# Kernel optimization log

Hardware: AMD Instinct MI355X
Metric: run time of the kernel (lower is better)

Reference implementation:

```python
import jax, jax.numpy as jnp
import numpy as np

INPUT_DIM = 128
RESERVOIR = 4096
SR = 0.95
SCALE_IN = 1.0
LEAK = 0.3
DENSITY = 0.1
T = 2048


def setup_inputs() -> dict:
    key = jax.random.key(0)
    kx, kin, kw, km = jax.random.split(key, 4)
    x = jax.random.normal(kx, (T, INPUT_DIM), dtype=jnp.float32)
    # input weights ~ U(-scale_in, scale_in)
    W_in = jax.random.uniform(kin, (RESERVOIR, INPUT_DIM), minval=-SCALE_IN, maxval=SCALE_IN, dtype=jnp.float32)
    # sparse recurrent weights ~ U(-1,1) with given density, rescaled to target
    # spectral radius via circular-law estimate rho ~= sqrt(N * density * Var),
    # Var(U(-1,1)) = 1/3 (avoids an O(N^3) eig at setup; same math structure).
    W_dense = jax.random.uniform(kw, (RESERVOIR, RESERVOIR), minval=-1.0, maxval=1.0, dtype=jnp.float32)
    mask = (jax.random.uniform(km, (RESERVOIR, RESERVOIR)) < DENSITY).astype(jnp.float32)
    rho_est = float(np.sqrt(RESERVOIR * DENSITY / 3.0))
    W = W_dense * mask * (SR / rho_est)
    return {"x": x, "W_in": W_in, "W": W}


def reference(x, W_in, W):
    # Leaky-integrator ESN: h_t = (1-a) h_{t-1} + a * tanh(W_in x_t + W h_{t-1})
    a = jnp.float32(LEAK)
    h0 = jnp.zeros((W.shape[0],), dtype=x.dtype)

    def step(h, xt):
        pre = W_in @ xt + W @ h
        h_new = (1.0 - a) * h + a * jnp.tanh(pre)
        return h_new, h_new

    _, states = jax.lax.scan(step, h0, x)
    # torch.stack(states) -> [T, reservoir]
    return states
```

## Files before the change

kernel.cpp:

```cpp
#include <hip/hip_runtime.h>

#define N 4096
#define IN_DIM 128
#define T_STEPS 2048
#define KSLOTS 576
#define CHUNKS (KSLOTS / 64)
#define NBLOCKS 256
#define NTHREADS 512
#define ROWS_PER_WAVE 2
#define ROWS_PER_BLOCK (ROWS_PER_WAVE * (NTHREADS / 64))
#define SENTINEL_BITS 0x7FC00001u

typedef float f32x4 __attribute__((ext_vector_type(4)));

__global__ void init_sentinel(float* __restrict__ out) {
    const size_t i = (size_t)blockIdx.x * blockDim.x + threadIdx.x;
    __hip_atomic_store(&out[i], __uint_as_float(SENTINEL_BITS),
                       __ATOMIC_RELAXED, __HIP_MEMORY_SCOPE_AGENT);
}

__global__ void build_ell(const float* __restrict__ W,
                          float* __restrict__ vals,
                          unsigned short* __restrict__ cols) {
    __shared__ float sval[KSLOTS];
    __shared__ unsigned short scol[KSLOTS];
    __shared__ float slot_val[KSLOTS];
    __shared__ unsigned short slot_col[KSLOTS];
    __shared__ int chunk_fill[CHUNKS];
    __shared__ int cnt;

    const int r = blockIdx.x;
    const int tid = threadIdx.x;
    if (tid == 0) cnt = 0;
    if (tid < CHUNKS) chunk_fill[tid] = 0;
    __syncthreads();

    const float* wrow = W + (size_t)r * N;
    for (int j = tid; j < N; j += blockDim.x) {
        float w = wrow[j];
        if (w != 0.0f) {
            int p = atomicAdd(&cnt, 1);
            if (p < KSLOTS) { sval[p] = w; scol[p] = (unsigned short)j; }
        }
    }
    __syncthreads();
    for (int j = tid; j < KSLOTS; j += blockDim.x) { slot_val[j] = 0.0f; slot_col[j] = 0; }
    __syncthreads();

    if (tid < 32) {
        int k = 0;
        const int n = (cnt < KSLOTS) ? cnt : KSLOTS;
        for (int p = 0; p < n; ++p) {
            int c = scol[p];
            if ((c & 31) == tid) {
                int ch0 = (k + tid) % CHUNKS;
                for (int probe = 0; probe < CHUNKS; ++probe) {
                    int cc = ch0 + probe; if (cc >= CHUNKS) cc -= CHUNKS;
                    int pos = atomicAdd(&chunk_fill[cc], 1);
                    if (pos < 64) {
                        slot_val[cc * 64 + pos] = sval[p];
                        slot_col[cc * 64 + pos] = (unsigned short)c;
                        break;
                    }
                }
                ++k;
            }
        }
    }
    __syncthreads();

    float* vrow = vals + (size_t)r * KSLOTS;
    unsigned short* crow = cols + (size_t)r * KSLOTS;
    for (int j = tid; j < KSLOTS; j += blockDim.x) { vrow[j] = slot_val[j]; crow[j] = slot_col[j]; }
}

__device__ __forceinline__ f32x4 load_coherent_x4(const float* p) {
    f32x4 v;
    asm volatile("global_load_dwordx4 %0, %1, off sc0 sc1\n\t"
                 "s_waitcnt vmcnt(0)"
                 : "=v"(v) : "v"(p) : "memory");
    return v;
}

__device__ __forceinline__ void load_coherent_x4_pair(const float* p0, const float* p1,
                                                      f32x4* v0, f32x4* v1) {
    f32x4 a, b;
    asm volatile("global_load_dwordx4 %0, %2, off sc0 sc1\n\t"
                 "global_load_dwordx4 %1, %3, off sc0 sc1\n\t"
                 "s_waitcnt vmcnt(0)"
                 : "=v"(a), "=v"(b) : "v"(p0), "v"(p1) : "memory");
    *v0 = a; *v1 = b;
}

__device__ __forceinline__ void store_coherent_x4(float* p, f32x4 v) {
    asm volatile("global_store_dwordx4 %0, %1, off sc0 sc1"
                 :: "v"(p), "v"(v) : "memory");
}

__device__ __forceinline__ bool granule_not_ready(f32x4 hv) {
    return (__float_as_uint(hv.x) == SENTINEL_BITS) |
           (__float_as_uint(hv.y) == SENTINEL_BITS) |
           (__float_as_uint(hv.z) == SENTINEL_BITS) |
           (__float_as_uint(hv.w) == SENTINEL_BITS);
}

__device__ __forceinline__ float fast_tanh(float v) {
    float ax = __builtin_fabsf(v);
    float e  = __builtin_amdgcn_exp2f(ax * 2.88539008177793f);
    float r  = 1.0f - 2.0f * __builtin_amdgcn_rcpf(e + 1.0f);
    return __builtin_copysignf(r, v);
}

__device__ __forceinline__ float dpp_reduce_add(float v) {
    int t;
    t = __builtin_amdgcn_update_dpp(0, __float_as_int(v), 0x111, 0xf, 0xf, true);
    v += __int_as_float(t);
    t = __builtin_amdgcn_update_dpp(0, __float_as_int(v), 0x112, 0xf, 0xf, true);
    v += __int_as_float(t);
    t = __builtin_amdgcn_update_dpp(0, __float_as_int(v), 0x114, 0xf, 0xf, true);
    v += __int_as_float(t);
    t = __builtin_amdgcn_update_dpp(0, __float_as_int(v), 0x118, 0xf, 0xf, true);
    v += __int_as_float(t);
    t = __builtin_amdgcn_update_dpp(0, __float_as_int(v), 0x142, 0xa, 0xf, true);
    v += __int_as_float(t);
    t = __builtin_amdgcn_update_dpp(0, __float_as_int(v), 0x143, 0xc, 0xf, true);
    v += __int_as_float(t);
    return v;
}

__global__ void __launch_bounds__(NTHREADS, 1) esn_steps(
    const float* __restrict__ x,
    const float* __restrict__ W_in,
    const float* __restrict__ vals,
    const unsigned short* __restrict__ cols,
    float* __restrict__ out) {

    __shared__ float h_lds[N];
    __shared__ __align__(16) float hout[ROWS_PER_BLOCK];

    const int tid  = threadIdx.x;
    const int lane = tid & 63;
    const int wave = tid >> 6;
    const int blockBase = blockIdx.x * ROWS_PER_BLOCK;
    const int base = blockBase + wave * ROWS_PER_WAVE;

    float w0[ROWS_PER_WAVE], w1[ROWS_PER_WAVE];
    #pragma unroll
    for (int j = 0; j < ROWS_PER_WAVE; ++j) {
        w0[j] = W_in[(base + j) * IN_DIM + lane];
        w1[j] = W_in[(base + j) * IN_DIM + 64 + lane];
    }

    float rv[ROWS_PER_WAVE][CHUNKS];
    int   rc[ROWS_PER_WAVE][CHUNKS];
    #pragma unroll
    for (int j = 0; j < ROWS_PER_WAVE; ++j) {
        const float* vp = vals + (size_t)(base + j) * KSLOTS;
        const unsigned short* cp = cols + (size_t)(base + j) * KSLOTS;
        #pragma unroll
        for (int i = 0; i < CHUNKS; ++i) {
            rv[j][i] = vp[(i << 6) + lane];
            rc[j][i] = ((int)cp[(i << 6) + lane]) << 2;
        }
    }

    const int i4 = tid << 2;

    for (int t = 0; t < T_STEPS; ++t) {
        const float xa = x[t * IN_DIM + lane];
        const float xb = x[t * IN_DIM + 64 + lane];

        f32x4 hv0, hv1;
        if (t > 0) {
            const float* a0 = out + (size_t)(t - 1) * N + i4;
            const float* a1 = a0 + (NTHREADS * 4);
            __builtin_amdgcn_s_sleep(8);
            load_coherent_x4_pair(a0, a1, &hv0, &hv1);
            if (granule_not_ready(hv0) | granule_not_ready(hv1)) {
                __builtin_amdgcn_s_sleep(1);
                load_coherent_x4_pair(a0, a1, &hv0, &hv1);
                if (granule_not_ready(hv0) | granule_not_ready(hv1)) {
                    __builtin_amdgcn_s_sleep(2);
                    load_coherent_x4_pair(a0, a1, &hv0, &hv1);
                    while (granule_not_ready(hv0) | granule_not_ready(hv1)) {
                        __builtin_amdgcn_s_sleep(4);
                        load_coherent_x4_pair(a0, a1, &hv0, &hv1);
                    }
                }
            }
        } else {
            hv0 = (f32x4)(0.0f);
            hv1 = (f32x4)(0.0f);
        }
        ((f32x4*)h_lds)[tid] = hv0;
        ((f32x4*)h_lds)[tid + NTHREADS] = hv1;
        __syncthreads();

        float acc[ROWS_PER_WAVE];
        #pragma unroll
        for (int j = 0; j < ROWS_PER_WAVE; ++j) acc[j] = w0[j] * xa + w1[j] * xb;

        #pragma unroll
        for (int j = 0; j < ROWS_PER_WAVE; ++j) {
            #pragma unroll
            for (int i = 0; i < CHUNKS; ++i) {
                acc[j] += rv[j][i] * *(const float*)((const char*)h_lds + rc[j][i]);
            }
        }

        acc[0] = dpp_reduce_add(acc[0]);
        acc[1] = dpp_reduce_add(acc[1]);

        if (lane == 63) {
            float hp0 = h_lds[base + 0];
            float hp1 = h_lds[base + 1];
            hout[wave * ROWS_PER_WAVE + 0] = 0.7f * hp0 + 0.3f * fast_tanh(acc[0]);
            hout[wave * ROWS_PER_WAVE + 1] = 0.7f * hp1 + 0.3f * fast_tanh(acc[1]);
        }
        __syncthreads();

        if (tid < ROWS_PER_BLOCK / 4) {
            f32x4 hv4 = ((const f32x4*)hout)[tid];
            store_coherent_x4(out + (size_t)t * N + blockBase + (tid << 2), hv4);
        }
    }
}

extern "C" void kernel_launch(void* const* d_in, const int* in_sizes, int n_in,
                              void* d_out, int out_size, void* d_ws, size_t ws_size,
                              hipStream_t stream) {
    const float* x    = (const float*)d_in[0];
    const float* W_in = (const float*)d_in[1];
    const float* W    = (const float*)d_in[2];
    float* out = (float*)d_out;

    char* ws = (char*)d_ws;
    float* vals = (float*)ws;
    unsigned short* cols = (unsigned short*)(ws + (size_t)N * KSLOTS * 4);

    init_sentinel<<<(T_STEPS * N) / 1024, 1024, 0, stream>>>(out);
    build_ell<<<N, 256, 0, stream>>>(W, vals, cols);

    void* args[] = {(void*)&x, (void*)&W_in, (void*)&vals, (void*)&cols, (void*)&out};
    hipLaunchCooperativeKernel((void*)esn_steps, dim3(NBLOCKS), dim3(NTHREADS),
                               args, 0, stream);
}
```

Baseline: 3.148 ms.

## Exchange recurrent state between blocks as fp16 in workspace buffer

Adds a half-precision copy of each step's hidden state in workspace, which blocks poll and read instead of the fp32 output. This halves the bytes every block must fetch per step across the grid-wide dependency, cutting the coherent-load latency on the critical path. The fp32 output is still written with plain stores. It adds rounding error to the recurrent input, and the fast path is only taken when the workspace is large enough.

```diff
diff --git a/kernel.cpp b/kernel.cpp
--- a/kernel.cpp
+++ b/kernel.cpp
@@ -1,4 +1,5 @@
 #include <hip/hip_runtime.h>
+#include <hip/hip_fp16.h>
 
 #define N 4096
 #define IN_DIM 128
@@ -10,13 +11,18 @@
 #define ROWS_PER_WAVE 2
 #define ROWS_PER_BLOCK (ROWS_PER_WAVE * (NTHREADS / 64))
 #define SENTINEL_BITS 0x7FC00001u
+#define H16_SENT 0x7E01u
+#define H16_BYTES_PER_STEP (N * 2)
 
 typedef float f32x4 __attribute__((ext_vector_type(4)));
 
-__global__ void init_sentinel(float* __restrict__ out) {
+__global__ void init_sentinel(float* __restrict__ out, unsigned int* __restrict__ h16) {
     const size_t i = (size_t)blockIdx.x * blockDim.x + threadIdx.x;
     __hip_atomic_store(&out[i], __uint_as_float(SENTINEL_BITS),
                        __ATOMIC_RELAXED, __HIP_MEMORY_SCOPE_AGENT);
+    if (h16 && i < ((size_t)T_STEPS * H16_BYTES_PER_STEP / 4))
+        __hip_atomic_store(&h16[i], (H16_SENT << 16) | H16_SENT,
+                           __ATOMIC_RELAXED, __HIP_MEMORY_SCOPE_AGENT);
 }
 
 __global__ void build_ell(const float* __restrict__ W,
@@ -104,6 +110,15 @@
            (__float_as_uint(hv.w) == SENTINEL_BITS);
 }
 
+__device__ __forceinline__ bool h16_not_ready(f32x4 hv) {
+    unsigned int w0 = __float_as_uint(hv.x), w1 = __float_as_uint(hv.y);
+    unsigned int w2 = __float_as_uint(hv.z), w3 = __float_as_uint(hv.w);
+    return ((w0 & 0xFFFFu) == H16_SENT) | ((w0 >> 16) == H16_SENT) |
+           ((w1 & 0xFFFFu) == H16_SENT) | ((w1 >> 16) == H16_SENT) |
+           ((w2 & 0xFFFFu) == H16_SENT) | ((w2 >> 16) == H16_SENT) |
+           ((w3 & 0xFFFFu) == H16_SENT) | ((w3 >> 16) == H16_SENT);
+}
+
 __device__ __forceinline__ float fast_tanh(float v) {
     float ax = __builtin_fabsf(v);
     float e  = __builtin_amdgcn_exp2f(ax * 2.88539008177793f);
@@ -133,7 +148,9 @@
     const float* __restrict__ W_in,
     const float* __restrict__ vals,
     const unsigned short* __restrict__ cols,
-    float* __restrict__ out) {
+    float* __restrict__ out,
+    char* __restrict__ h16,
+    int use_h16) {
 
     __shared__ float h_lds[N];
     __shared__ __align__(16) float hout[ROWS_PER_BLOCK];
@@ -170,30 +187,63 @@
         const float xa = x[t * IN_DIM + lane];
         const float xb = x[t * IN_DIM + 64 + lane];
 
-        f32x4 hv0, hv1;
         if (t > 0) {
-            const float* a0 = out + (size_t)(t - 1) * N + i4;
-            const float* a1 = a0 + (NTHREADS * 4);
-            __builtin_amdgcn_s_sleep(8);
-            load_coherent_x4_pair(a0, a1, &hv0, &hv1);
-            if (granule_not_ready(hv0) | granule_not_ready(hv1)) {
-                __builtin_amdgcn_s_sleep(1);
+            if (use_h16) {
+                const float* addr = (const float*)(h16 +
+                    (size_t)(t - 1) * H16_BYTES_PER_STEP + (tid << 4));
+                f32x4 hv;
+                __builtin_amdgcn_s_sleep(8);
+                hv = load_coherent_x4(addr);
+                if (h16_not_ready(hv)) {
+                    __builtin_amdgcn_s_sleep(1);
+                    hv = load_coherent_x4(addr);
+                    if (h16_not_ready(hv)) {
+                        __builtin_amdgcn_s_sleep(2);
+                        hv = load_coherent_x4(addr);
+                        while (h16_not_ready(hv)) {
+                            __builtin_amdgcn_s_sleep(4);
+                            hv = load_coherent_x4(addr);
+                        }
+                    }
+                }
+                unsigned int u0 = __float_as_uint(hv.x), u1 = __float_as_uint(hv.y);
+                unsigned int u2 = __float_as_uint(hv.z), u3 = __float_as_uint(hv.w);
+                f32x4 lo, hi;
+                lo.x = __half2float(__ushort_as_half((unsigned short)(u0 & 0xFFFFu)));
+                lo.y = __half2float(__ushort_as_half((unsigned short)(u0 >> 16)));
+                lo.z = __half2float(__ushort_as_half((unsigned short)(u1 & 0xFFFFu)));
+                lo.w = __half2float(__ushort_as_half((unsigned short)(u1 >> 16)));
+                hi.x = __half2float(__ushort_as_half((unsigned short)(u2 & 0xFFFFu)));
+                hi.y = __half2float(__ushort_as_half((unsigned short)(u2 >> 16)));
+                hi.z = __half2float(__ushort_as_half((unsigned short)(u3 & 0xFFFFu)));
+                hi.w = __half2float(__ushort_as_half((unsigned short)(u3 >> 16)));
+                ((f32x4*)h_lds)[tid * 2]     = lo;
+                ((f32x4*)h_lds)[tid * 2 + 1] = hi;
+            } else {
+                f32x4 hv0, hv1;
+                const float* a0 = out + (size_t)(t - 1) * N + i4;
+                const float* a1 = a0 + (NTHREADS * 4);
+                __builtin_amdgcn_s_sleep(8);
                 load_coherent_x4_pair(a0, a1, &hv0, &hv1);
                 if (granule_not_ready(hv0) | granule_not_ready(hv1)) {
-                    __builtin_amdgcn_s_sleep(2);
+                    __builtin_amdgcn_s_sleep(1);
                     load_coherent_x4_pair(a0, a1, &hv0, &hv1);
-                    while (granule_not_ready(hv0) | granule_not_ready(hv1)) {
-                        __builtin_amdgcn_s_sleep(4);
+                    if (granule_not_ready(hv0) | granule_not_ready(hv1)) {
+                        __builtin_amdgcn_s_sleep(2);
                         load_coherent_x4_pair(a0, a1, &hv0, &hv1);
+                        while (granule_not_ready(hv0) | granule_not_ready(hv1)) {
+                            __builtin_amdgcn_s_sleep(4);
+                            load_coherent_x4_pair(a0, a1, &hv0, &hv1);
+                        }
                     }
                 }
+                ((f32x4*)h_lds)[tid] = hv0;
+                ((f32x4*)h_lds)[tid + NTHREADS] = hv1;
             }
         } else {
-            hv0 = (f32x4)(0.0f);
-            hv1 = (f32x4)(0.0f);
-        }
-        ((f32x4*)h_lds)[tid] = hv0;
-        ((f32x4*)h_lds)[tid + NTHREADS] = hv1;
+            ((f32x4*)h_lds)[tid * 2]     = (f32x4)(0.0f);
+            ((f32x4*)h_lds)[tid * 2 + 1] = (f32x4)(0.0f);
+        }
         __syncthreads();
 
         float acc[ROWS_PER_WAVE];
@@ -219,9 +269,30 @@
         }
         __syncthreads();
 
-        if (tid < ROWS_PER_BLOCK / 4) {
-            f32x4 hv4 = ((const f32x4*)hout)[tid];
-            store_coherent_x4(out + (size_t)t * N + blockBase + (tid << 2), hv4);
+        if (use_h16) {
+            if (tid < 2) {
+                const float* hp = &hout[tid * 8];
+                __half2 p0 = __floats2half2_rn(hp[0], hp[1]);
+                __half2 p1 = __floats2half2_rn(hp[2], hp[3]);
+                __half2 p2 = __floats2half2_rn(hp[4], hp[5]);
+                __half2 p3 = __floats2half2_rn(hp[6], hp[7]);
+                f32x4 pk;
+                pk.x = __uint_as_float(*(unsigned int*)&p0);
+                pk.y = __uint_as_float(*(unsigned int*)&p1);
+                pk.z = __uint_as_float(*(unsigned int*)&p2);
+                pk.w = __uint_as_float(*(unsigned int*)&p3);
+                store_coherent_x4((float*)(h16 + (size_t)t * H16_BYTES_PER_STEP
+                                           + blockIdx.x * 32 + (tid << 4)), pk);
+            }
+            if (tid < ROWS_PER_BLOCK / 4) {
+                f32x4 hv4 = ((const f32x4*)hout)[tid];
+                *(((f32x4*)(out + (size_t)t * N + blockBase)) + tid) = hv4;
+            }
+        } else {
+            if (tid < ROWS_PER_BLOCK / 4) {
+                f32x4 hv4 = ((const f32x4*)hout)[tid];
+                store_coherent_x4(out + (size_t)t * N + blockBase + (tid << 2), hv4);
+            }
         }
     }
 }
@@ -238,10 +309,17 @@
     float* vals = (float*)ws;
     unsigned short* cols = (unsigned short*)(ws + (size_t)N * KSLOTS * 4);
 
-    init_sentinel<<<(T_STEPS * N) / 1024, 1024, 0, stream>>>(out);
+    const size_t ell_bytes = (size_t)N * KSLOTS * 6;
+    const size_t h16_bytes = (size_t)T_STEPS * H16_BYTES_PER_STEP;
+    int use_h16 = (ws_size >= ell_bytes + h16_bytes) ? 1 : 0;
+    char* h16 = use_h16 ? (ws + ell_bytes) : nullptr;
+
+    init_sentinel<<<(T_STEPS * N) / 1024, 1024, 0, stream>>>(
+        out, (unsigned int*)h16);
     build_ell<<<N, 256, 0, stream>>>(W, vals, cols);
 
-    void* args[] = {(void*)&x, (void*)&W_in, (void*)&vals, (void*)&cols, (void*)&out};
+    void* args[] = {(void*)&x, (void*)&W_in, (void*)&vals, (void*)&cols,
+                    (void*)&out, (void*)&h16, (void*)&use_h16};
     hipLaunchCooperativeKernel((void*)esn_steps, dim3(NBLOCKS), dim3(NTHREADS),
                                args, 0, stream);
 }
```

Result: no change. 3.178 ms (+1.0%).
